# Kernel tuning notes

Measured on AMD Instinct MI355X. Metric: run time of the kernel, lower is better.

## Reference

```python
import jax, jax.numpy as jnp
import numpy as np


def setup_inputs() -> dict:
    key = jax.random.key(0)
    k1, k2 = jax.random.split(key)
    b, t, d = 4, 2048, 1024
    x = jax.random.normal(k1, (b, t, d), dtype=jnp.float32)
    # torch Linear weight has shape [out_features, in_features] = [3*d, d]
    W_qkv = jax.random.normal(k2, (3 * d, d), dtype=jnp.float32) * (2.0 / (d + 3 * d)) ** 0.5
    return {"x": x, "W_qkv": W_qkv}


def reference(x, W_qkv):
    b, t, d = x.shape
    scale = d ** -0.5
    qkv = jnp.einsum('btd,ed->bte', x, W_qkv)          # [b, t, 3d]
    # rearrange 'b t (d k) -> k b t d' with k=3: last axis splits as (d, 3)
    qkv = qkv.reshape(b, t, d, 3)
    q, k, v = qkv[..., 0], qkv[..., 1], qkv[..., 2]     # each [b, t, d]
    scores = jnp.einsum('bid,bjd->bij', q, k) * scale   # [b, t, t]
    attn = jax.nn.softmax(scores, axis=-1)
    return jnp.einsum('bij,bjd->bid', attn, v)          # [b, t, d]
```

## Files before the change

kernel.cpp:

```cpp
#include <hip/hip_runtime.h>
#include <math.h>

#define NBATCH 4
#define TDIM 2048
#define DDIM 1024

typedef __attribute__((ext_vector_type(8))) short short8;
typedef __attribute__((ext_vector_type(4))) float floatx4;
typedef __attribute__((ext_vector_type(8))) unsigned short ushort8;
typedef __attribute__((ext_vector_type(4))) unsigned short ushort4v;

__device__ __forceinline__ unsigned short f2bf(float f) {
  unsigned int u = __float_as_uint(f);
  u += 0x7fffu + ((u >> 16) & 1u);
  return (unsigned short)(u >> 16);
}

__device__ __forceinline__ void gload_lds16(const ushort* g, ushort* l) {
  __builtin_amdgcn_global_load_lds(
      (const __attribute__((address_space(1))) void*)g,
      (__attribute__((address_space(3))) void*)l, 16, 0, 0);
}

__device__ __forceinline__ void mfma_gemm_core(
    const ushort* __restrict__ Abase, const ushort* __restrict__ Bbase,
    int lda, int ldb, int K, ushort* As, ushort* Bs, floatx4 acc[4][4]) {
  const int tid = threadIdx.x;
  const int wave = tid >> 6;
  const int lane = tid & 63;
  const int l15 = lane & 15;
  const int quad = lane >> 4;
  const int wm = wave >> 1, wn = wave & 1;

  const int srow = wave * 32 + (lane >> 3);
  const int schunk = (lane & 7) ^ ((lane >> 3) & 7);
  const ushort* ag = Abase + (size_t)srow * lda + schunk * 8;
  const ushort* bg = Bbase + (size_t)srow * ldb + schunk * 8;
  ushort* al = As + wave * 32 * 64;
  ushort* bl = Bs + wave * 32 * 64;

  const int slot = quad ^ (l15 & 7);
  const int abase = (wm * 64 + l15) * 64 + slot * 8;
  const int bbase = (wn * 64 + l15) * 64 + slot * 8;

  for (int kt = 0; kt < K; kt += 64) {
#pragma unroll
    for (int i = 0; i < 4; ++i) {
      gload_lds16(ag + kt + (size_t)(8 * i) * lda, al + 8 * i * 64);
      gload_lds16(bg + kt + (size_t)(8 * i) * ldb, bl + 8 * i * 64);
    }
    __syncthreads();
#pragma unroll
    for (int g = 0; g < 2; ++g) {
      const int ab = abase ^ (g * 32);
      const int bb = bbase ^ (g * 32);
      short8 af[4], bfr[4];
#pragma unroll
      for (int t = 0; t < 4; ++t) {
        af[t] = *(const short8*)&As[ab + t * 1024];
        bfr[t] = *(const short8*)&Bs[bb + t * 1024];
      }
#pragma unroll
      for (int i = 0; i < 4; ++i)
#pragma unroll
        for (int j = 0; j < 4; ++j)
          acc[i][j] =
              __builtin_amdgcn_mfma_f32_16x16x32_bf16(af[i], bfr[j], acc[i][j], 0, 0, 0);
    }
    __syncthreads();
  }
}

__global__ __launch_bounds__(256) void convert_xw(
    const float* __restrict__ x, const float* __restrict__ W,
    ushort* __restrict__ xb, ushort* __restrict__ wb) {
  const int bid = blockIdx.x;
  if (bid < 8192) {
    const size_t i = (size_t)bid * 256 + threadIdx.x;
    float4 v = reinterpret_cast<const float4*>(x)[i];
    ushort4v h = {f2bf(v.x), f2bf(v.y), f2bf(v.z), f2bf(v.w)};
    reinterpret_cast<ushort4v*>(xb)[i] = h;
  } else {
    const int e = bid - 8192;
    const int c = e % 3, ii = e / 3;
    const float scale = (c == 0) ? 0.03125f : 1.0f;
    const float4 v = reinterpret_cast<const float4*>(W + (size_t)e * DDIM)[threadIdx.x];
    ushort4v h = {f2bf(v.x * scale), f2bf(v.y * scale), f2bf(v.z * scale),
                  f2bf(v.w * scale)};
    reinterpret_cast<ushort4v*>(wb + (size_t)(c * DDIM + ii) * DDIM)[threadIdx.x] = h;
  }
}

__global__ __launch_bounds__(256, 3) void qkv_gemm(
    const ushort* __restrict__ xb, const ushort* __restrict__ wb,
    ushort* __restrict__ qb, ushort* __restrict__ kb, ushort* __restrict__ vt) {
  __shared__ __align__(16) ushort As[128 * 64];
  __shared__ __align__(16) ushort Bs[128 * 64];
  const int m0 = blockIdx.y * 128;
  const int n0 = blockIdx.x * 128;
  floatx4 acc[4][4];
  const floatx4 z4 = {0.f, 0.f, 0.f, 0.f};
#pragma unroll
  for (int i = 0; i < 4; ++i)
#pragma unroll
    for (int j = 0; j < 4; ++j) acc[i][j] = z4;

  mfma_gemm_core(xb + (size_t)m0 * DDIM, wb + (size_t)n0 * DDIM, DDIM, DDIM,
                 DDIM, As, Bs, acc);

  const int tid = threadIdx.x;
  const int wave = tid >> 6, lane = tid & 63;
  const int l15 = lane & 15, quad = lane >> 4;
  const int wm = wave >> 1, wn = wave & 1;

  if (n0 < 2 * DDIM) {
    ushort* dst = (n0 < DDIM) ? qb : kb;
    const int cb = (n0 < DDIM) ? n0 : n0 - DDIM;
#pragma unroll
    for (int i = 0; i < 4; ++i) {
      const int rbase = m0 + wm * 64 + i * 16 + quad * 4;
#pragma unroll
      for (int j = 0; j < 4; ++j) {
        const int col = cb + wn * 64 + j * 16 + l15;
#pragma unroll
        for (int r = 0; r < 4; ++r)
          dst[(size_t)(rbase + r) * DDIM + col] = f2bf(acc[i][j][r]);
      }
    }
  } else {
#pragma unroll
    for (int i = 0; i < 4; ++i) {
      const int row = m0 + wm * 64 + i * 16 + quad * 4;
      const int b = row >> 11, t = row & (TDIM - 1);
#pragma unroll
      for (int j = 0; j < 4; ++j) {
        const int d = (n0 - 2 * DDIM) + wn * 64 + j * 16 + l15;
        ushort4v pk = {f2bf(acc[i][j][0]), f2bf(acc[i][j][1]),
                       f2bf(acc[i][j][2]), f2bf(acc[i][j][3])};
        *reinterpret_cast<ushort4v*>(&vt[(size_t)((b << 10) + d) * TDIM + t]) = pk;
      }
    }
  }
}

__global__ __launch_bounds__(256, 3) void score_gemm(
    const ushort* __restrict__ qb, const ushort* __restrict__ kb,
    ushort* __restrict__ Sb, float* __restrict__ lpart) {
  __shared__ __align__(16) ushort As[128 * 64];
  __shared__ __align__(16) ushort Bs[128 * 64];
  const int z = blockIdx.z;
  const int m0 = blockIdx.y * 128;
  const int n0 = blockIdx.x * 128;
  floatx4 acc[4][4];
  const floatx4 z4 = {0.f, 0.f, 0.f, 0.f};
#pragma unroll
  for (int i = 0; i < 4; ++i)
#pragma unroll
    for (int j = 0; j < 4; ++j) acc[i][j] = z4;

  mfma_gemm_core(qb + ((size_t)z * TDIM + m0) * DDIM,
                 kb + ((size_t)z * TDIM + n0) * DDIM, DDIM, DDIM, DDIM, As, Bs,
                 acc);

  const int tid = threadIdx.x;
  const int wave = tid >> 6, lane = tid & 63;
  const int l15 = lane & 15, quad = lane >> 4;
  const int wm = wave >> 1, wn = wave & 1;

  ushort* S = Sb + (size_t)z * TDIM * TDIM;
#pragma unroll
  for (int i = 0; i < 4; ++i)
#pragma unroll
    for (int j = 0; j < 4; ++j)
#pragma unroll
      for (int r = 0; r < 4; ++r) acc[i][j][r] = __expf(acc[i][j][r]);

#pragma unroll
  for (int i = 0; i < 4; ++i) {
    const int rbase = m0 + wm * 64 + i * 16 + quad * 4;
#pragma unroll
    for (int j = 0; j < 4; ++j) {
      const int col = n0 + wn * 64 + j * 16 + l15;
#pragma unroll
      for (int r = 0; r < 4; ++r)
        S[(size_t)(rbase + r) * TDIM + col] = f2bf(acc[i][j][r]);
    }
  }

  float* sums = reinterpret_cast<float*>(As);
  __syncthreads();
#pragma unroll
  for (int i = 0; i < 4; ++i) {
#pragma unroll
    for (int r = 0; r < 4; ++r) {
      float s = acc[i][0][r] + acc[i][1][r] + acc[i][2][r] + acc[i][3][r];
#pragma unroll
      for (int off = 8; off > 0; off >>= 1) s += __shfl_down(s, off, 16);
      if (l15 == 0) sums[(wm * 64 + i * 16 + quad * 4 + r) * 2 + wn] = s;
    }
  }
  __syncthreads();
  if (tid < 128)
    lpart[((size_t)z * 16 + blockIdx.x) * TDIM + m0 + tid] =
        sums[tid * 2] + sums[tid * 2 + 1];
}

__global__ __launch_bounds__(256, 3) void pv_gemm(
    const ushort* __restrict__ Pb, const ushort* __restrict__ vt,
    const float* __restrict__ lpart, float* __restrict__ out) {
  __shared__ __align__(16) ushort As[128 * 64];
  __shared__ __align__(16) ushort Bs[128 * 64];
  const int z = blockIdx.z;
  const int m0 = blockIdx.y * 128;
  const int n0 = blockIdx.x * 128;
  floatx4 acc[4][4];
  const floatx4 z4 = {0.f, 0.f, 0.f, 0.f};
#pragma unroll
  for (int i = 0; i < 4; ++i)
#pragma unroll
    for (int j = 0; j < 4; ++j) acc[i][j] = z4;

  mfma_gemm_core(Pb + (size_t)z * TDIM * TDIM + (size_t)m0 * TDIM,
                 vt + (size_t)z * DDIM * TDIM + (size_t)n0 * TDIM, TDIM, TDIM,
                 TDIM, As, Bs, acc);

  const int tid = threadIdx.x;
  const int wave = tid >> 6, lane = tid & 63;
  const int l15 = lane & 15, quad = lane >> 4;
  const int wm = wave >> 1, wn = wave & 1;

  float* linv = reinterpret_cast<float*>(As);
  __syncthreads();
  if (tid < 128) {
    float s = 0.f;
#pragma unroll
    for (int nb = 0; nb < 16; ++nb)
      s += lpart[((size_t)z * 16 + nb) * TDIM + m0 + tid];
    linv[tid] = 1.0f / s;
  }
  __syncthreads();

  float* O = out + (size_t)z * TDIM * DDIM;
#pragma unroll
  for (int i = 0; i < 4; ++i) {
    const int rl = wm * 64 + i * 16 + quad * 4;
    const int rbase = m0 + rl;
#pragma unroll
    for (int j = 0; j < 4; ++j) {
      const int col = n0 + wn * 64 + j * 16 + l15;
#pragma unroll
      for (int r = 0; r < 4; ++r)
        O[(size_t)(rbase + r) * DDIM + col] = acc[i][j][r] * linv[rl + r];
    }
  }
}

extern "C" void kernel_launch(void* const* d_in, const int* in_sizes, int n_in,
                              void* d_out, int out_size, void* d_ws, size_t ws_size,
                              hipStream_t stream) {
  const float* x = (const float*)d_in[0];
  const float* W = (const float*)d_in[1];
  float* out = (float*)d_out;

  ushort* ws = (ushort*)d_ws;
  const size_t n_x = (size_t)NBATCH * TDIM * DDIM;
  const size_t n_w = (size_t)3 * DDIM * DDIM;
  ushort* xb = ws;
  ushort* wb = xb + n_x;
  ushort* qb = wb + n_w;
  ushort* kb = qb + n_x;
  ushort* vt = kb + n_x;
  ushort* Sb = vt + n_x;
  float* lpart = (float*)(Sb + (size_t)NBATCH * TDIM * TDIM);

  convert_xw<<<dim3(8192 + 3 * DDIM), 256, 0, stream>>>(x, W, xb, wb);
  qkv_gemm<<<dim3(3 * DDIM / 128, NBATCH * TDIM / 128), 256, 0, stream>>>(
      xb, wb, qb, kb, vt);
  score_gemm<<<dim3(TDIM / 128, TDIM / 128, NBATCH), 256, 0, stream>>>(qb, kb,
                                                                       Sb, lpart);
  pv_gemm<<<dim3(DDIM / 128, TDIM / 128, NBATCH), 256, 0, stream>>>(Sb, vt,
                                                                    lpart, out);
}
```

Before: 240.0 us.

## Use 256x256 double-buffered 8-wave MFMA core for QKV and score GEMMs

Adds a new GEMM core with 256x256 block tiles, 8 waves, and double-buffered LDS. Each K-step is split into four phases that issue the next tile's global-to-LDS loads while running MFMAs, using explicit vmcnt waits, barriers and setprio. The QKV and score GEMMs switch to this core, and the softmax partial-sum layout changes to 8 column blocks, with pv_gemm updated to match. This targets better operand reuse and load/compute overlap, at the cost of 128KB of LDS per block, many accumulator registers, and fewer blocks for the score GEMM grid.

```diff
diff --git a/kernel.cpp b/kernel.cpp
--- a/kernel.cpp
+++ b/kernel.cpp
@@ -7,7 +7,6 @@
 
 typedef __attribute__((ext_vector_type(8))) short short8;
 typedef __attribute__((ext_vector_type(4))) float floatx4;
-typedef __attribute__((ext_vector_type(8))) unsigned short ushort8;
 typedef __attribute__((ext_vector_type(4))) unsigned short ushort4v;
 
 __device__ __forceinline__ unsigned short f2bf(float f) {
@@ -68,6 +67,103 @@
               __builtin_amdgcn_mfma_f32_16x16x32_bf16(af[i], bfr[j], acc[i][j], 0, 0, 0);
     }
     __syncthreads();
+  }
+}
+
+__device__ __forceinline__ void stage_B_half(const ushort* B, int ldb, int kt,
+                                             ushort* Bs, int h, int w, int lane) {
+#pragma unroll
+  for (int i = 0; i < 2; ++i) {
+    const int rb = h * 128 + w * 16 + 8 * i;
+    const int r = rb + (lane >> 3);
+    const int c = (lane & 7) ^ ((lane >> 3) & 7);
+    gload_lds16(B + (size_t)r * ldb + kt + c * 8, Bs + rb * 64);
+  }
+}
+
+__device__ __forceinline__ void stage_A_half(const ushort* A, int lda, int kt,
+                                             ushort* As, int mh, int w, int lane) {
+#pragma unroll
+  for (int i = 0; i < 2; ++i) {
+    const int g = w * 2 + i;
+    const int rb = mh * 64 + (g & 7) * 8 + (g >> 3) * 128;
+    const int r = rb + (lane >> 3);
+    const int c = (lane & 7) ^ ((lane >> 3) & 7);
+    gload_lds16(A + (size_t)r * lda + kt + c * 8, As + rb * 64);
+  }
+}
+
+__device__ __forceinline__ void mfma_core256(
+    const ushort* __restrict__ A, const ushort* __restrict__ B, int lda,
+    int ldb, int K, ushort* As0, ushort* As1, ushort* Bs0, ushort* Bs1,
+    floatx4 acc[8][4]) {
+  const int tid = threadIdx.x;
+  const int w = tid >> 6, lane = tid & 63;
+  const int l15 = lane & 15, quad = lane >> 4;
+  const int wm = w >> 2, wn = w & 3;
+  const int slot = (quad ^ (l15 & 7)) * 8;
+  const int abase = (wm * 128 + l15) * 64 + slot;
+  const int bbase = (wn * 64 + l15) * 64 + slot;
+  const int NT = K >> 6;
+
+  stage_B_half(B, ldb, 0, Bs0, 0, w, lane);
+  stage_B_half(B, ldb, 0, Bs0, 1, w, lane);
+  stage_A_half(A, lda, 0, As0, 0, w, lane);
+  stage_A_half(A, lda, 0, As0, 1, w, lane);
+  asm volatile("s_waitcnt vmcnt(2)" ::: "memory");
+  __builtin_amdgcn_s_barrier();
+
+  const ushort* cA = As0;
+  const ushort* cB = Bs0;
+  ushort* nA = As1;
+  ushort* nB = Bs1;
+
+#pragma unroll 1
+  for (int t = 0; t < NT; ++t) {
+    const int ktn = (t + 1) << 6;
+    const bool pf = (t + 1 < NT);
+#pragma unroll
+    for (int p = 0; p < 4; ++p) {
+      const int mh = p >> 1, nh = p & 1;
+      short8 af[4][2], bfm[2][2];
+#pragma unroll
+      for (int f = 0; f < 4; ++f)
+#pragma unroll
+        for (int g = 0; g < 2; ++g)
+          af[f][g] = *(const short8*)&cA[(abase + mh * 4096 + f * 1024) ^ (g * 32)];
+#pragma unroll
+      for (int f = 0; f < 2; ++f)
+#pragma unroll
+        for (int g = 0; g < 2; ++g)
+          bfm[f][g] = *(const short8*)&cB[(bbase + nh * 2048 + f * 1024) ^ (g * 32)];
+      if (pf) {
+        if (p == 0)      stage_B_half(B, ldb, ktn, nB, 0, w, lane);
+        else if (p == 1) stage_B_half(B, ldb, ktn, nB, 1, w, lane);
+        else if (p == 2) stage_A_half(A, lda, ktn, nA, 0, w, lane);
+        else             stage_A_half(A, lda, ktn, nA, 1, w, lane);
+      }
+      __builtin_amdgcn_s_barrier();
+      __builtin_amdgcn_s_setprio(1);
+#pragma unroll
+      for (int f = 0; f < 4; ++f)
+#pragma unroll
+        for (int fj = 0; fj < 2; ++fj)
+#pragma unroll
+          for (int g = 0; g < 2; ++g)
+            acc[mh * 4 + f][nh * 2 + fj] =
+                __builtin_amdgcn_mfma_f32_16x16x32_bf16(
+                    af[f][g], bfm[fj][g], acc[mh * 4 + f][nh * 2 + fj], 0, 0, 0);
+      __builtin_amdgcn_s_setprio(0);
+      if (p == 1) {
+        if (pf) asm volatile("s_waitcnt vmcnt(4)" ::: "memory");
+        else    asm volatile("s_waitcnt vmcnt(0)" ::: "memory");
+      } else if (p == 3) {
+        asm volatile("s_waitcnt vmcnt(2)" ::: "memory");
+      }
+      __builtin_amdgcn_s_barrier();
+    }
+    ushort* tmp = nA; nA = (ushort*)cA; cA = tmp;
+    tmp = nB; nB = (ushort*)cB; cB = tmp;
   }
 }
 
@@ -91,34 +187,34 @@
   }
 }
 
-__global__ __launch_bounds__(256, 3) void qkv_gemm(
+__global__ __launch_bounds__(512, 2) void qkv_gemm8(
     const ushort* __restrict__ xb, const ushort* __restrict__ wb,
     ushort* __restrict__ qb, ushort* __restrict__ kb, ushort* __restrict__ vt) {
-  __shared__ __align__(16) ushort As[128 * 64];
-  __shared__ __align__(16) ushort Bs[128 * 64];
-  const int m0 = blockIdx.y * 128;
-  const int n0 = blockIdx.x * 128;
-  floatx4 acc[4][4];
+  __shared__ __align__(16) ushort As0[256 * 64], As1[256 * 64];
+  __shared__ __align__(16) ushort Bs0[256 * 64], Bs1[256 * 64];
+  const int m0 = blockIdx.y * 256;
+  const int n0 = blockIdx.x * 256;
+  floatx4 acc[8][4];
   const floatx4 z4 = {0.f, 0.f, 0.f, 0.f};
 #pragma unroll
-  for (int i = 0; i < 4; ++i)
+  for (int i = 0; i < 8; ++i)
 #pragma unroll
     for (int j = 0; j < 4; ++j) acc[i][j] = z4;
 
-  mfma_gemm_core(xb + (size_t)m0 * DDIM, wb + (size_t)n0 * DDIM, DDIM, DDIM,
-                 DDIM, As, Bs, acc);
-
-  const int tid = threadIdx.x;
-  const int wave = tid >> 6, lane = tid & 63;
+  mfma_core256(xb + (size_t)m0 * DDIM, wb + (size_t)n0 * DDIM, DDIM, DDIM,
+               DDIM, As0, As1, Bs0, Bs1, acc);
+
+  const int tid = threadIdx.x;
+  const int w = tid >> 6, lane = tid & 63;
   const int l15 = lane & 15, quad = lane >> 4;
-  const int wm = wave >> 1, wn = wave & 1;
+  const int wm = w >> 2, wn = w & 3;
 
   if (n0 < 2 * DDIM) {
     ushort* dst = (n0 < DDIM) ? qb : kb;
     const int cb = (n0 < DDIM) ? n0 : n0 - DDIM;
 #pragma unroll
-    for (int i = 0; i < 4; ++i) {
-      const int rbase = m0 + wm * 64 + i * 16 + quad * 4;
+    for (int i = 0; i < 8; ++i) {
+      const int rbase = m0 + wm * 128 + i * 16 + quad * 4;
 #pragma unroll
       for (int j = 0; j < 4; ++j) {
         const int col = cb + wn * 64 + j * 16 + l15;
@@ -129,8 +225,8 @@
     }
   } else {
 #pragma unroll
-    for (int i = 0; i < 4; ++i) {
-      const int row = m0 + wm * 64 + i * 16 + quad * 4;
+    for (int i = 0; i < 8; ++i) {
+      const int row = m0 + wm * 128 + i * 16 + quad * 4;
       const int b = row >> 11, t = row & (TDIM - 1);
 #pragma unroll
       for (int j = 0; j < 4; ++j) {
@@ -143,41 +239,41 @@
   }
 }
 
-__global__ __launch_bounds__(256, 3) void score_gemm(
+__global__ __launch_bounds__(512, 2) void score_gemm8(
     const ushort* __restrict__ qb, const ushort* __restrict__ kb,
     ushort* __restrict__ Sb, float* __restrict__ lpart) {
-  __shared__ __align__(16) ushort As[128 * 64];
-  __shared__ __align__(16) ushort Bs[128 * 64];
+  __shared__ __align__(16) ushort As0[256 * 64], As1[256 * 64];
+  __shared__ __align__(16) ushort Bs0[256 * 64], Bs1[256 * 64];
   const int z = blockIdx.z;
-  const int m0 = blockIdx.y * 128;
-  const int n0 = blockIdx.x * 128;
-  floatx4 acc[4][4];
+  const int m0 = blockIdx.y * 256;
+  const int n0 = blockIdx.x * 256;
+  floatx4 acc[8][4];
   const floatx4 z4 = {0.f, 0.f, 0.f, 0.f};
 #pragma unroll
-  for (int i = 0; i < 4; ++i)
+  for (int i = 0; i < 8; ++i)
 #pragma unroll
     for (int j = 0; j < 4; ++j) acc[i][j] = z4;
 
-  mfma_gemm_core(qb + ((size_t)z * TDIM + m0) * DDIM,
-                 kb + ((size_t)z * TDIM + n0) * DDIM, DDIM, DDIM, DDIM, As, Bs,
-                 acc);
-
-  const int tid = threadIdx.x;
-  const int wave = tid >> 6, lane = tid & 63;
+  mfma_core256(qb + ((size_t)z * TDIM + m0) * DDIM,
+               kb + ((size_t)z * TDIM + n0) * DDIM, DDIM, DDIM, DDIM, As0, As1,
+               Bs0, Bs1, acc);
+
+  const int tid = threadIdx.x;
+  const int w = tid >> 6, lane = tid & 63;
   const int l15 = lane & 15, quad = lane >> 4;
-  const int wm = wave >> 1, wn = wave & 1;
+  const int wm = w >> 2, wn = w & 3;
 
   ushort* S = Sb + (size_t)z * TDIM * TDIM;
 #pragma unroll
-  for (int i = 0; i < 4; ++i)
+  for (int i = 0; i < 8; ++i)
 #pragma unroll
     for (int j = 0; j < 4; ++j)
 #pragma unroll
       for (int r = 0; r < 4; ++r) acc[i][j][r] = __expf(acc[i][j][r]);
 
 #pragma unroll
-  for (int i = 0; i < 4; ++i) {
-    const int rbase = m0 + wm * 64 + i * 16 + quad * 4;
+  for (int i = 0; i < 8; ++i) {
+    const int rbase = m0 + wm * 128 + i * 16 + quad * 4;
 #pragma unroll
     for (int j = 0; j < 4; ++j) {
       const int col = n0 + wn * 64 + j * 16 + l15;
@@ -187,22 +283,22 @@
     }
   }
 
-  float* sums = reinterpret_cast<float*>(As);
+  float* sums = reinterpret_cast<float*>(As0);
   __syncthreads();
 #pragma unroll
-  for (int i = 0; i < 4; ++i) {
+  for (int i = 0; i < 8; ++i) {
 #pragma unroll
     for (int r = 0; r < 4; ++r) {
       float s = acc[i][0][r] + acc[i][1][r] + acc[i][2][r] + acc[i][3][r];
 #pragma unroll
       for (int off = 8; off > 0; off >>= 1) s += __shfl_down(s, off, 16);
-      if (l15 == 0) sums[(wm * 64 + i * 16 + quad * 4 + r) * 2 + wn] = s;
+      if (l15 == 0) sums[(wm * 128 + i * 16 + quad * 4 + r) * 4 + wn] = s;
     }
   }
   __syncthreads();
-  if (tid < 128)
-    lpart[((size_t)z * 16 + blockIdx.x) * TDIM + m0 + tid] =
-        sums[tid * 2] + sums[tid * 2 + 1];
+  if (tid < 256)
+    lpart[((size_t)z * 8 + blockIdx.x) * TDIM + m0 + tid] =
+        sums[tid * 4] + sums[tid * 4 + 1] + sums[tid * 4 + 2] + sums[tid * 4 + 3];
 }
 
 __global__ __launch_bounds__(256, 3) void pv_gemm(
@@ -234,8 +330,8 @@
   if (tid < 128) {
     float s = 0.f;
 #pragma unroll
-    for (int nb = 0; nb < 16; ++nb)
-      s += lpart[((size_t)z * 16 + nb) * TDIM + m0 + tid];
+    for (int nb = 0; nb < 8; ++nb)
+      s += lpart[((size_t)z * 8 + nb) * TDIM + m0 + tid];
     linv[tid] = 1.0f / s;
   }
   __syncthreads();
@@ -274,10 +370,10 @@
   float* lpart = (float*)(Sb + (size_t)NBATCH * TDIM * TDIM);
 
   convert_xw<<<dim3(8192 + 3 * DDIM), 256, 0, stream>>>(x, W, xb, wb);
-  qkv_gemm<<<dim3(3 * DDIM / 128, NBATCH * TDIM / 128), 256, 0, stream>>>(
+  qkv_gemm8<<<dim3(3 * DDIM / 256, NBATCH * TDIM / 256), 512, 0, stream>>>(
       xb, wb, qb, kb, vt);
-  score_gemm<<<dim3(TDIM / 128, TDIM / 128, NBATCH), 256, 0, stream>>>(qb, kb,
-                                                                       Sb, lpart);
+  score_gemm8<<<dim3(TDIM / 256, TDIM / 256, NBATCH), 512, 0, stream>>>(
+      qb, kb, Sb, lpart);
   pv_gemm<<<dim3(DDIM / 128, TDIM / 128, NBATCH), 256, 0, stream>>>(Sb, vt,
                                                                     lpart, out);
 }
```

Result: slower. 251.3 us (+4.7%).
